# Kernel optimization log

Measured on AMD Instinct MI355X. Metric: run time of the kernel, lower is better.

The kernel has to match this reference:

```python
import jax, jax.numpy as jnp
import numpy as np
from functools import partial

V, BS, L, H, C = 50257, 1024, 6, 12, 768
HD = C // H

def _ln(x, w, b):
    mu = jnp.mean(x, axis=-1, keepdims=True)
    var = jnp.var(x, axis=-1, keepdims=True)
    return (x - mu) * jax.lax.rsqrt(var + 1e-5) * w + b

def setup_inputs() -> dict:
    key = jax.random.key(0)
    ks = jax.random.split(key, 12)
    s = 0.02
    inp = {
        "idx": jax.random.randint(ks[0], (4, 1024), 0, V, dtype=jnp.int32),
        "wte": jax.random.normal(ks[1], (V, C), jnp.float32) * s,
        "wpe": jax.random.normal(ks[2], (BS, C), jnp.float32) * s,
        # per-block stacked params; linear weights stored [in, out]
        "ln1_w": jnp.ones((L, C)), "ln1_b": jnp.zeros((L, C)),
        "attn_w": jax.random.normal(ks[3], (L, C, 3 * C), jnp.float32) * s,
        "attn_b": jnp.zeros((L, 3 * C)),
        "proj_w": jax.random.normal(ks[4], (L, C, C), jnp.float32) * s,
        "proj_b": jnp.zeros((L, C)),
        "ln2_w": jnp.ones((L, C)), "ln2_b": jnp.zeros((L, C)),
        "fc_w": jax.random.normal(ks[5], (L, C, 4 * C), jnp.float32) * s,
        "fc_b": jnp.zeros((L, 4 * C)),
        "fc2_w": jax.random.normal(ks[6], (L, 4 * C, C), jnp.float32) * s,
        "fc2_b": jnp.zeros((L, C)),
        "lnf_w": jnp.ones((C,)), "lnf_b": jnp.zeros((C,)),
    }
    return inp

def _forward(idx, wte, wpe, ln1_w, ln1_b, attn_w, attn_b, proj_w, proj_b,
             ln2_w, ln2_b, fc_w, fc_b, fc2_w, fc2_b, lnf_w, lnf_b):
    B, T = idx.shape
    x = wte[idx] + wpe[:T]  # [B,T,C]
    causal = jnp.tril(jnp.ones((T, T), bool))  # [T,T]
    scale = 1.0 / np.sqrt(HD)
    neg_inf = jnp.finfo(x.dtype).min

    def block(x, p):
        l1w, l1b, aw, ab, pw, pb, l2w, l2b, fw, fb, f2w, f2b = p
        h = _ln(x, l1w, l1b)
        qkv = h @ aw + ab  # [B,T,3C]
        q, k, v = jnp.split(qkv, 3, axis=-1)
        q = q.reshape(B, T, H, HD)
        k = k.reshape(B, T, H, HD)
        v = v.reshape(B, T, H, HD)
        att = jnp.einsum('bqhd,bkhd->bhqk', q, k) * scale
        att = jnp.where(causal, att, neg_inf)
        att = jax.nn.softmax(att, axis=-1)
        y = jnp.einsum('bhqk,bkhd->bqhd', att, v).reshape(B, T, C)
        x = x + y @ pw + pb
        h = _ln(x, l2w, l2b)
        h = jax.nn.gelu(h @ fw + fb, approximate=False)  # torch nn.GELU default = exact
        x = x + h @ f2w + f2b
        return x, None

    params = (ln1_w, ln1_b, attn_w, attn_b, proj_w, proj_b,
              ln2_w, ln2_b, fc_w, fc_b, fc2_w, fc2_b)
    x, _ = jax.lax.scan(block, x, params)
    x = _ln(x, lnf_w, lnf_b)
    logits = x @ wte.T  # tied lm_head, no bias
    return logits

def reference(idx, wte, wpe, ln1_w, ln1_b, attn_w, attn_b, proj_w, proj_b,
              ln2_w, ln2_b, fc_w, fc_b, fc2_w, fc2_b, lnf_w, lnf_b):
    return _forward(idx, wte, wpe, ln1_w, ln1_b, attn_w, attn_b, proj_w, proj_b,
                    ln2_w, ln2_b, fc_w, fc_b, fc2_w, fc2_b, lnf_w, lnf_b)
```

## Files before the change

### kernel.cpp

```cpp
#include <hip/hip_runtime.h>

#define BT     4096
#define CDIM   768
#define NLAYER 6
#define NHEAD  12
#define VREAL  50257
#define VPAD   50432

typedef __bf16 bf16x8 __attribute__((ext_vector_type(8)));
typedef float  f32x4  __attribute__((ext_vector_type(4)));

__device__ __forceinline__ unsigned short f2bf(float f) {
    unsigned int u = __builtin_bit_cast(unsigned int, f);
    u += 0x7fffu + ((u >> 16) & 1u);
    return (unsigned short)(u >> 16);
}

__device__ __forceinline__ void swz_block(int &bx, int &by) {
    int gx = gridDim.x;
    int nwg = gx * gridDim.y;
    if ((nwg & 7) == 0) {
        int lin = by * gx + bx;
        int q = nwg >> 3;
        lin = (lin & 7) * q + (lin >> 3);
        bx = lin % gx;
        by = lin / gx;
    }
}

__global__ __launch_bounds__(256) void transpose_conv(
    const float* __restrict__ in, unsigned short* __restrict__ out, int K, int N)
{
    in  += (size_t)blockIdx.z * K * N;
    out += (size_t)blockIdx.z * K * N;
    __shared__ float t[32][33];
    int j0 = blockIdx.x * 32;
    int i0 = blockIdx.y * 32;
    int c = threadIdx.x;
    int r = threadIdx.y;
    #pragma unroll
    for (int rr = r; rr < 32; rr += 8)
        t[rr][c] = in[(size_t)(i0 + rr) * N + j0 + c];
    __syncthreads();
    #pragma unroll
    for (int rr = r; rr < 32; rr += 8)
        out[(size_t)(j0 + rr) * K + i0 + c] = f2bf(t[c][rr]);
}

__global__ __launch_bounds__(256) void wteconv(
    const float* __restrict__ wte, unsigned short* __restrict__ out)
{
    size_t e = ((size_t)blockIdx.x * 256 + threadIdx.x) * 4;
    int row = (int)(e / CDIM);
    int col = (int)(e % CDIM);
    ushort4 o;
    if (row < VREAL) {
        float4 v = *(const float4*)(wte + (size_t)row * CDIM + col);
        o.x = f2bf(v.x); o.y = f2bf(v.y); o.z = f2bf(v.z); o.w = f2bf(v.w);
    } else {
        o.x = 0; o.y = 0; o.z = 0; o.w = 0;
    }
    *(ushort4*)(out + e) = o;
}

__global__ __launch_bounds__(256) void embed_kernel(
    const int* __restrict__ idx, const float* __restrict__ wte,
    const float* __restrict__ wpe, float* __restrict__ x)
{
    int row = blockIdx.x;
    int t = row & 1023;
    int id = idx[row];
    const float* s = wte + (size_t)id * CDIM;
    const float* p = wpe + (size_t)t * CDIM;
    float* o = x + (size_t)row * CDIM;
    for (int c = threadIdx.x; c < CDIM; c += 256) o[c] = s[c] + p[c];
}

__global__ __launch_bounds__(256) void ln_kernel(
    const float* __restrict__ x, const float* __restrict__ w,
    const float* __restrict__ b, unsigned short* __restrict__ out)
{
    int row = blockIdx.x * 4 + (threadIdx.x >> 6);
    int lane = threadIdx.x & 63;
    const float* xp = x + (size_t)row * CDIM;
    float v[12];
    float s = 0.f, sq = 0.f;
    #pragma unroll
    for (int j = 0; j < 12; ++j) {
        float t = xp[j * 64 + lane];
        v[j] = t; s += t; sq += t * t;
    }
    #pragma unroll
    for (int o = 32; o > 0; o >>= 1) {
        s  += __shfl_xor(s, o, 64);
        sq += __shfl_xor(sq, o, 64);
    }
    float mu  = s * (1.f / CDIM);
    float var = sq * (1.f / CDIM) - mu * mu;
    float rs  = rsqrtf(var + 1e-5f);
    unsigned short* op = out + (size_t)row * CDIM;
    #pragma unroll
    for (int j = 0; j < 12; ++j) {
        int c = j * 64 + lane;
        op[c] = f2bf((v[j] - mu) * rs * w[c] + b[c]);
    }
}

template<int MODE>
__global__ __launch_bounds__(256) void gemm_kernel(
    const unsigned short* __restrict__ A, const unsigned short* __restrict__ Bt,
    const float* __restrict__ bias, const float* __restrict__ resid,
    float* __restrict__ outF, unsigned short* __restrict__ outB,
    unsigned short* __restrict__ qout, unsigned short* __restrict__ kout,
    unsigned short* __restrict__ vtout,
    int K, int Nout)
{
    __shared__ alignas(16) unsigned short As[2][4096];
    __shared__ alignas(16) unsigned short Bs[2][4096];
    const int tid  = threadIdx.x;
    const int wv   = tid >> 6;
    const int lane = tid & 63;
    int bx = blockIdx.x, by = blockIdx.y;
    swz_block(bx, by);
    const int m0 = bx * 128;
    const int n0 = by * 128;
    const int wr = wv >> 1, wc = wv & 1;
    const int srow = lane >> 2;
    const int skk  = (lane & 3) * 8;
    const int fr = lane & 15;
    const int fk = (lane >> 4) * 8;

    auto stage = [&](int k0, int bb) {
        #pragma unroll
        for (int j = 0; j < 2; ++j) {
            int row = j * 64 + wv * 16 + srow;
            const unsigned short* ga = A  + (size_t)(m0 + row) * K + k0 + skk;
            const unsigned short* gb = Bt + (size_t)(n0 + row) * K + k0 + skk;
            __builtin_amdgcn_global_load_lds(
                (const __attribute__((address_space(1))) unsigned int*)ga,
                (__attribute__((address_space(3))) unsigned int*)&As[bb][j * 2048 + wv * 512],
                16, 0, 0);
            __builtin_amdgcn_global_load_lds(
                (const __attribute__((address_space(1))) unsigned int*)gb,
                (__attribute__((address_space(3))) unsigned int*)&Bs[bb][j * 2048 + wv * 512],
                16, 0, 0);
        }
    };

    f32x4 acc[4][4];
    #pragma unroll
    for (int i = 0; i < 4; ++i)
        #pragma unroll
        for (int j = 0; j < 4; ++j) acc[i][j] = f32x4{0.f, 0.f, 0.f, 0.f};

    stage(0, 0);
    __syncthreads();

    const int nt = K >> 5;
    for (int t = 0; t < nt; ++t) {
        const int cb = t & 1;
        if (t + 1 < nt) stage((t + 1) << 5, cb ^ 1);
        bf16x8 a[4], bb[4];
        #pragma unroll
        for (int m = 0; m < 4; ++m)
            a[m] = *(const bf16x8*)&As[cb][(wr * 64 + m * 16 + fr) * 32 + fk];
        #pragma unroll
        for (int n = 0; n < 4; ++n)
            bb[n] = *(const bf16x8*)&Bs[cb][(wc * 64 + n * 16 + fr) * 32 + fk];
        #pragma unroll
        for (int m = 0; m < 4; ++m)
            #pragma unroll
            for (int n = 0; n < 4; ++n)
                acc[m][n] = __builtin_amdgcn_mfma_f32_16x16x32_bf16(
                    a[m], bb[n], acc[m][n], 0, 0, 0);
        __syncthreads();
    }

    const int colb = n0 + wc * 64 + fr;
    const int rowb = m0 + wr * 64 + (lane >> 4) * 4;
    #pragma unroll
    for (int m = 0; m < 4; ++m) {
        #pragma unroll
        for (int n = 0; n < 4; ++n) {
            int col = colb + n * 16;
            int which = col / 768;
            int hh = (col - which * 768) >> 6;
            int dd = col & 63;
            #pragma unroll
            for (int r = 0; r < 4; ++r) {
                int row = rowb + m * 16 + r;
                float v = acc[m][n][r];
                if (MODE == 1) {
                    outF[(size_t)row * Nout + col] =
                        resid[(size_t)row * Nout + col] + v + bias[col];
                } else if (MODE == 2) {
                    float u = v + bias[col];
                    float g = 0.5f * u * (1.f + erff(u * 0.70710678118654752f));
                    outB[(size_t)row * Nout + col] = f2bf(g);
                } else if (MODE == 4) {
                    int bb2 = row >> 10, tt = row & 1023;
                    unsigned short val = f2bf(v + bias[col]);
                    if (which == 0)
                        qout[(((size_t)bb2 * NHEAD + hh) * 1024 + tt) * 64 + dd] = val;
                    else if (which == 1)
                        kout[(((size_t)bb2 * NHEAD + hh) * 1024 + tt) * 64 + dd] = val;
                    else
                        vtout[(((size_t)bb2 * NHEAD + hh) * 64 + dd) * 1024 + tt] = val;
                }
            }
        }
    }
}

__global__ __launch_bounds__(512, 2) void gemm256_kernel(
    const unsigned short* __restrict__ A, const unsigned short* __restrict__ Bt,
    float* __restrict__ outF, int K, int Nout)
{
    __shared__ alignas(16) unsigned short ldsA[2][16384];
    __shared__ alignas(16) unsigned short ldsB[2][16384];
    const int tid  = threadIdx.x;
    const int wid  = tid >> 6;
    const int lane = tid & 63;
    int bx = blockIdx.x, by = blockIdx.y;
    swz_block(bx, by);
    const int m0 = bx * 256;
    const int n0 = by * 256;
    const int wm = wid >> 2;
    const int wn = wid & 3;
    const int srow = wid * 8 + (lane >> 3);
    const int scol = (lane & 7) * 8;
    const int fr = lane & 15;
    const int fg = lane >> 4;

    auto stage = [&](int kt, int bb) {
        const int k0 = kt * 64;
        #pragma unroll
        for (int j = 0; j < 4; ++j) {
            const unsigned short* ga = A  + (size_t)(m0 + j * 64 + srow) * K + k0 + scol;
            const unsigned short* gb = Bt + (size_t)(n0 + j * 64 + srow) * K + k0 + scol;
            __builtin_amdgcn_global_load_lds(
                (const __attribute__((address_space(1))) unsigned int*)ga,
                (__attribute__((address_space(3))) unsigned int*)&ldsA[bb][j * 4096 + wid * 512],
                16, 0, 0);
            __builtin_amdgcn_global_load_lds(
                (const __attribute__((address_space(1))) unsigned int*)gb,
                (__attribute__((address_space(3))) unsigned int*)&ldsB[bb][j * 4096 + wid * 512],
                16, 0, 0);
        }
    };

    f32x4 acc[8][4];
    #pragma unroll
    for (int i = 0; i < 8; ++i)
        #pragma unroll
        for (int j = 0; j < 4; ++j) acc[i][j] = f32x4{0.f, 0.f, 0.f, 0.f};

    stage(0, 0);
    __syncthreads();

    const int nt = K >> 6;
    for (int t = 0; t < nt; ++t) {
        const int cb = t & 1;
        if (t + 1 < nt) stage(t + 1, cb ^ 1);
        #pragma unroll
        for (int ks = 0; ks < 2; ++ks) {
            bf16x8 a[8], b[4];
            #pragma unroll
            for (int m = 0; m < 8; ++m)
                a[m] = *(const bf16x8*)&ldsA[cb][(wm * 128 + m * 16 + fr) * 64 + ks * 32 + fg * 8];
            #pragma unroll
            for (int n = 0; n < 4; ++n)
                b[n] = *(const bf16x8*)&ldsB[cb][(wn * 64 + n * 16 + fr) * 64 + ks * 32 + fg * 8];
            #pragma unroll
            for (int m = 0; m < 8; ++m)
                #pragma unroll
                for (int n = 0; n < 4; ++n)
                    acc[m][n] = __builtin_amdgcn_mfma_f32_16x16x32_bf16(
                        a[m], b[n], acc[m][n], 0, 0, 0);
        }
        __syncthreads();
    }

    const int colb = n0 + wn * 64 + fr;
    const int rowb = m0 + wm * 128 + fg * 4;
    #pragma unroll
    for (int m = 0; m < 8; ++m) {
        #pragma unroll
        for (int n = 0; n < 4; ++n) {
            int col = colb + n * 16;
            if (col < Nout) {
                #pragma unroll
                for (int r = 0; r < 4; ++r) {
                    int row = rowb + m * 16 + r;
                    outF[(size_t)row * Nout + col] = acc[m][n][r];
                }
            }
        }
    }
}

__global__ __launch_bounds__(256) void attn_mfma_kernel(
    const unsigned short* __restrict__ qb, const unsigned short* __restrict__ kb,
    const unsigned short* __restrict__ vtb, unsigned short* __restrict__ y)
{
    __shared__ alignas(16) unsigned short Ps[4][16][72];
    const int qt = 15 - blockIdx.x;
    const int h = blockIdx.y, b = blockIdx.z;
    const int w = threadIdx.x >> 6, lane = threadIdx.x & 63;
    const int fr = lane & 15;
    const int fg = lane >> 4;
    const size_t bh = (size_t)(b * NHEAD + h);
    const unsigned short* Qb = qb  + bh * 1024 * 64;
    const unsigned short* Kb = kb  + bh * 1024 * 64;
    const unsigned short* Vt = vtb + bh * 64 * 1024;
    const int q0 = qt * 64 + w * 16;

    bf16x8 aq[2];
    aq[0] = *(const bf16x8*)(Qb + (size_t)(q0 + fr) * 64 + fg * 8);
    aq[1] = *(const bf16x8*)(Qb + (size_t)(q0 + fr) * 64 + 32 + fg * 8);

    f32x4 o[4];
    #pragma unroll
    for (int c = 0; c < 4; ++c) o[c] = f32x4{0.f, 0.f, 0.f, 0.f};
    float m[4], l[4];
    #pragma unroll
    for (int r = 0; r < 4; ++r) { m[r] = -1e30f; l[r] = 0.f; }

    for (int kt = 0; kt <= qt; ++kt) {
        const unsigned short* Kt = Kb + (size_t)kt * 64 * 64;
        f32x4 s[4];
        #pragma unroll
        for (int c = 0; c < 4; ++c) {
            bf16x8 bk0 = *(const bf16x8*)(Kt + (size_t)(c * 16 + fr) * 64 + fg * 8);
            bf16x8 bk1 = *(const bf16x8*)(Kt + (size_t)(c * 16 + fr) * 64 + 32 + fg * 8);
            s[c] = f32x4{0.f, 0.f, 0.f, 0.f};
            s[c] = __builtin_amdgcn_mfma_f32_16x16x32_bf16(aq[0], bk0, s[c], 0, 0, 0);
            s[c] = __builtin_amdgcn_mfma_f32_16x16x32_bf16(aq[1], bk1, s[c], 0, 0, 0);
        }
        float sc[4][4];
        #pragma unroll
        for (int c = 0; c < 4; ++c)
            #pragma unroll
            for (int r = 0; r < 4; ++r) {
                float v = s[c][r] * 0.125f;
                if (kt == qt && (kt * 64 + c * 16 + fr) > (q0 + fg * 4 + r))
                    v = -1e30f;
                sc[c][r] = v;
            }
        #pragma unroll
        for (int r = 0; r < 4; ++r) {
            float tm = fmaxf(fmaxf(sc[0][r], sc[1][r]), fmaxf(sc[2][r], sc[3][r]));
            tm = fmaxf(tm, __shfl_xor(tm, 1, 64));
            tm = fmaxf(tm, __shfl_xor(tm, 2, 64));
            tm = fmaxf(tm, __shfl_xor(tm, 4, 64));
            tm = fmaxf(tm, __shfl_xor(tm, 8, 64));
            float mn = fmaxf(m[r], tm);
            float corr = __expf(m[r] - mn);
            m[r] = mn;
            float ps = 0.f;
            #pragma unroll
            for (int c = 0; c < 4; ++c) {
                float p = __expf(sc[c][r] - mn);
                sc[c][r] = p;
                ps += p;
            }
            ps += __shfl_xor(ps, 1, 64);
            ps += __shfl_xor(ps, 2, 64);
            ps += __shfl_xor(ps, 4, 64);
            ps += __shfl_xor(ps, 8, 64);
            l[r] = l[r] * corr + ps;
            #pragma unroll
            for (int c = 0; c < 4; ++c) o[c][r] *= corr;
            #pragma unroll
            for (int c = 0; c < 4; ++c)
                Ps[w][fg * 4 + r][c * 16 + fr] = f2bf(sc[c][r]);
        }
        asm volatile("s_waitcnt lgkmcnt(0)" ::: "memory");
        bf16x8 ap0 = *(const bf16x8*)&Ps[w][fr][fg * 8];
        bf16x8 ap1 = *(const bf16x8*)&Ps[w][fr][32 + fg * 8];
        #pragma unroll
        for (int c = 0; c < 4; ++c) {
            const unsigned short* vb = Vt + (size_t)(c * 16 + fr) * 1024 + kt * 64;
            bf16x8 bv0 = *(const bf16x8*)(vb + fg * 8);
            bf16x8 bv1 = *(const bf16x8*)(vb + 32 + fg * 8);
            o[c] = __builtin_amdgcn_mfma_f32_16x16x32_bf16(ap0, bv0, o[c], 0, 0, 0);
            o[c] = __builtin_amdgcn_mfma_f32_16x16x32_bf16(ap1, bv1, o[c], 0, 0, 0);
        }
        asm volatile("s_waitcnt lgkmcnt(0)" ::: "memory");
    }

    float inv[4];
    #pragma unroll
    for (int r = 0; r < 4; ++r) inv[r] = 1.f / l[r];
    #pragma unroll
    for (int c = 0; c < 4; ++c)
        #pragma unroll
        for (int r = 0; r < 4; ++r) {
            int q = q0 + fg * 4 + r;
            y[((size_t)(b * 1024 + q)) * CDIM + h * 64 + c * 16 + fr] =
                f2bf(o[c][r] * inv[r]);
        }
}

extern "C" void kernel_launch(void* const* d_in, const int* in_sizes, int n_in,
                              void* d_out, int out_size, void* d_ws, size_t ws_size,
                              hipStream_t stream) {
    (void)in_sizes; (void)n_in; (void)out_size; (void)ws_size;
    const int*   idx   = (const int*)  d_in[0];
    const float* wte   = (const float*)d_in[1];
    const float* wpe   = (const float*)d_in[2];
    const float* ln1w  = (const float*)d_in[3];
    const float* ln1b  = (const float*)d_in[4];
    const float* attnw = (const float*)d_in[5];
    const float* attnb = (const float*)d_in[6];
    const float* projw = (const float*)d_in[7];
    const float* projb = (const float*)d_in[8];
    const float* ln2w  = (const float*)d_in[9];
    const float* ln2b  = (const float*)d_in[10];
    const float* fcw   = (const float*)d_in[11];
    const float* fcb   = (const float*)d_in[12];
    const float* fc2w  = (const float*)d_in[13];
    const float* fc2b  = (const float*)d_in[14];
    const float* lnfw  = (const float*)d_in[15];
    const float* lnfb  = (const float*)d_in[16];
    float* out = (float*)d_out;

    char* ws = (char*)d_ws;
    size_t off = 0;
    auto alloc = [&](size_t bytes) {
        void* p = ws + off;
        off += (bytes + 255) & ~(size_t)255;
        return p;
    };
    float*          x      = (float*)         alloc((size_t)BT * CDIM * 4);
    unsigned short* hbuf   = (unsigned short*)alloc((size_t)BT * CDIM * 2);
    unsigned short* qbuf   = (unsigned short*)alloc((size_t)BT * CDIM * 2);
    unsigned short* kbuf   = (unsigned short*)alloc((size_t)BT * CDIM * 2);
    unsigned short* vtbuf  = (unsigned short*)alloc((size_t)BT * CDIM * 2);
    unsigned short* ybuf   = (unsigned short*)alloc((size_t)BT * CDIM * 2);
    unsigned short* fcact  = (unsigned short*)alloc((size_t)BT * 4 * CDIM * 2);
    unsigned short* wqkvT  = (unsigned short*)alloc((size_t)NLAYER * 3 * CDIM * CDIM * 2);
    unsigned short* wprojT = (unsigned short*)alloc((size_t)NLAYER * CDIM * CDIM * 2);
    unsigned short* wfcT   = (unsigned short*)alloc((size_t)NLAYER * 4 * CDIM * CDIM * 2);
    unsigned short* wfc2T  = (unsigned short*)alloc((size_t)NLAYER * 4 * CDIM * CDIM * 2);
    unsigned short* wteB   = (unsigned short*)alloc((size_t)VPAD * CDIM * 2);

    transpose_conv<<<dim3(3*CDIM/32,   CDIM/32, NLAYER), dim3(32,8), 0, stream>>>(attnw, wqkvT, CDIM, 3*CDIM);
    transpose_conv<<<dim3(  CDIM/32,   CDIM/32, NLAYER), dim3(32,8), 0, stream>>>(projw, wprojT, CDIM, CDIM);
    transpose_conv<<<dim3(4*CDIM/32,   CDIM/32, NLAYER), dim3(32,8), 0, stream>>>(fcw,  wfcT,  CDIM, 4*CDIM);
    transpose_conv<<<dim3(  CDIM/32, 4*CDIM/32, NLAYER), dim3(32,8), 0, stream>>>(fc2w, wfc2T, 4*CDIM, CDIM);
    wteconv<<<(VPAD * CDIM / 4) / 256, 256, 0, stream>>>(wte, wteB);
    embed_kernel<<<BT, 256, 0, stream>>>(idx, wte, wpe, x);

    for (int l = 0; l < NLAYER; ++l) {
        ln_kernel<<<BT/4, 256, 0, stream>>>(x, ln1w + l*CDIM, ln1b + l*CDIM, hbuf);
        gemm_kernel<4><<<dim3(BT/128, 3*CDIM/128), 256, 0, stream>>>(
            hbuf, wqkvT + (size_t)l*3*CDIM*CDIM, attnb + (size_t)l*3*CDIM,
            nullptr, nullptr, nullptr, qbuf, kbuf, vtbuf, CDIM, 3*CDIM);
        attn_mfma_kernel<<<dim3(16, NHEAD, 4), 256, 0, stream>>>(qbuf, kbuf, vtbuf, ybuf);
        gemm_kernel<1><<<dim3(BT/128, CDIM/128), 256, 0, stream>>>(
            ybuf, wprojT + (size_t)l*CDIM*CDIM, projb + (size_t)l*CDIM,
            x, x, nullptr, nullptr, nullptr, nullptr, CDIM, CDIM);
        ln_kernel<<<BT/4, 256, 0, stream>>>(x, ln2w + l*CDIM, ln2b + l*CDIM, hbuf);
        gemm_kernel<2><<<dim3(BT/128, 4*CDIM/128), 256, 0, stream>>>(
            hbuf, wfcT + (size_t)l*4*CDIM*CDIM, fcb + (size_t)l*4*CDIM,
            nullptr, nullptr, fcact, nullptr, nullptr, nullptr, CDIM, 4*CDIM);
        gemm_kernel<1><<<dim3(BT/128, CDIM/128), 256, 0, stream>>>(
            fcact, wfc2T + (size_t)l*4*CDIM*CDIM, fc2b + (size_t)l*CDIM,
            x, x, nullptr, nullptr, nullptr, nullptr, 4*CDIM, CDIM);
    }
    ln_kernel<<<BT/4, 256, 0, stream>>>(x, lnfw, lnfb, hbuf);
    gemm256_kernel<<<dim3(BT/256, VPAD/256), 512, 0, stream>>>(
        hbuf, wteB, out, CDIM, VREAL);
}
```

Before: 2.451 ms.

## Triple-buffer GEMM LDS staging with explicit vmcnt waits and prefetch distance two

Both GEMM kernels move from double-buffered to triple-buffered LDS staging and issue global-to-LDS loads two K-tiles ahead. The blanket __syncthreads is replaced by explicit s_waitcnt vmcnt counts, raw s_barrier, sched_barrier fences and s_setprio around the MFMA block. The 256 kernel also drops its K-tile from 64 to 32 to fit three buffers in LDS. The goal is to hide global load latency behind MFMA work, at the cost of one barrier per K-step for half as much work in the 256 kernel and hand-counted waits that must match the issued loads.

New measurement: 2.496 ms. No clear change (+1.8%).

```diff
diff --git a/kernel.cpp b/kernel.cpp
--- a/kernel.cpp
+++ b/kernel.cpp
@@ -14,6 +14,12 @@
     unsigned int u = __builtin_bit_cast(unsigned int, f);
     u += 0x7fffu + ((u >> 16) & 1u);
     return (unsigned short)(u >> 16);
+}
+
+__device__ __forceinline__ void gload16(const unsigned short* g, unsigned short* l) {
+    __builtin_amdgcn_global_load_lds(
+        (const __attribute__((address_space(1))) unsigned int*)g,
+        (__attribute__((address_space(3))) unsigned int*)l, 16, 0, 0);
 }
 
 __device__ __forceinline__ void swz_block(int &bx, int &by) {
@@ -115,8 +121,8 @@
     unsigned short* __restrict__ vtout,
     int K, int Nout)
 {
-    __shared__ alignas(16) unsigned short As[2][4096];
-    __shared__ alignas(16) unsigned short Bs[2][4096];
+    __shared__ alignas(16) unsigned short As[3][4096];
+    __shared__ alignas(16) unsigned short Bs[3][4096];
     const int tid  = threadIdx.x;
     const int wv   = tid >> 6;
     const int lane = tid & 63;
@@ -130,20 +136,13 @@
     const int fr = lane & 15;
     const int fk = (lane >> 4) * 8;
 
-    auto stage = [&](int k0, int bb) {
+    auto stage = [&](int t, int bb) {
+        const int k0 = t << 5;
         #pragma unroll
         for (int j = 0; j < 2; ++j) {
             int row = j * 64 + wv * 16 + srow;
-            const unsigned short* ga = A  + (size_t)(m0 + row) * K + k0 + skk;
-            const unsigned short* gb = Bt + (size_t)(n0 + row) * K + k0 + skk;
-            __builtin_amdgcn_global_load_lds(
-                (const __attribute__((address_space(1))) unsigned int*)ga,
-                (__attribute__((address_space(3))) unsigned int*)&As[bb][j * 2048 + wv * 512],
-                16, 0, 0);
-            __builtin_amdgcn_global_load_lds(
-                (const __attribute__((address_space(1))) unsigned int*)gb,
-                (__attribute__((address_space(3))) unsigned int*)&Bs[bb][j * 2048 + wv * 512],
-                16, 0, 0);
+            gload16(A  + (size_t)(m0 + row) * K + k0 + skk, &As[bb][j * 2048 + wv * 512]);
+            gload16(Bt + (size_t)(n0 + row) * K + k0 + skk, &Bs[bb][j * 2048 + wv * 512]);
         }
     };
 
@@ -153,13 +152,18 @@
         #pragma unroll
         for (int j = 0; j < 4; ++j) acc[i][j] = f32x4{0.f, 0.f, 0.f, 0.f};
 
+    const int nt = K >> 5;
     stage(0, 0);
-    __syncthreads();
-
-    const int nt = K >> 5;
+    if (nt > 1) stage(1, 1);
+
     for (int t = 0; t < nt; ++t) {
-        const int cb = t & 1;
-        if (t + 1 < nt) stage((t + 1) << 5, cb ^ 1);
+        const int cb = t % 3;
+        if (t + 2 < nt) stage(t + 2, (t + 2) % 3);
+        if (t + 2 < nt)      asm volatile("s_waitcnt vmcnt(8)" ::: "memory");
+        else if (t + 1 < nt) asm volatile("s_waitcnt vmcnt(4)" ::: "memory");
+        else                 asm volatile("s_waitcnt vmcnt(0)" ::: "memory");
+        __builtin_amdgcn_s_barrier();
+        __builtin_amdgcn_sched_barrier(0);
         bf16x8 a[4], bb[4];
         #pragma unroll
         for (int m = 0; m < 4; ++m)
@@ -167,13 +171,17 @@
         #pragma unroll
         for (int n = 0; n < 4; ++n)
             bb[n] = *(const bf16x8*)&Bs[cb][(wc * 64 + n * 16 + fr) * 32 + fk];
+        __builtin_amdgcn_s_setprio(1);
         #pragma unroll
         for (int m = 0; m < 4; ++m)
             #pragma unroll
             for (int n = 0; n < 4; ++n)
                 acc[m][n] = __builtin_amdgcn_mfma_f32_16x16x32_bf16(
                     a[m], bb[n], acc[m][n], 0, 0, 0);
-        __syncthreads();
+        __builtin_amdgcn_s_setprio(0);
+        asm volatile("s_waitcnt lgkmcnt(0)" ::: "memory");
+        __builtin_amdgcn_sched_barrier(0);
+        __builtin_amdgcn_s_barrier();
     }
 
     const int colb = n0 + wc * 64 + fr;
@@ -216,8 +224,8 @@
     const unsigned short* __restrict__ A, const unsigned short* __restrict__ Bt,
     float* __restrict__ outF, int K, int Nout)
 {
-    __shared__ alignas(16) unsigned short ldsA[2][16384];
-    __shared__ alignas(16) unsigned short ldsB[2][16384];
+    __shared__ alignas(16) unsigned short ldsA[3][8192];
+    __shared__ alignas(16) unsigned short ldsB[3][8192];
     const int tid  = threadIdx.x;
     const int wid  = tid >> 6;
     const int lane = tid & 63;
@@ -227,25 +235,20 @@
     const int n0 = by * 256;
     const int wm = wid >> 2;
     const int wn = wid & 3;
-    const int srow = wid * 8 + (lane >> 3);
-    const int scol = (lane & 7) * 8;
+    const int srow = wid * 16 + (lane >> 2);
+    const int scol = (lane & 3) * 8;
     const int fr = lane & 15;
     const int fg = lane >> 4;
 
-    auto stage = [&](int kt, int bb) {
-        const int k0 = kt * 64;
-        #pragma unroll
-        for (int j = 0; j < 4; ++j) {
-            const unsigned short* ga = A  + (size_t)(m0 + j * 64 + srow) * K + k0 + scol;
-            const unsigned short* gb = Bt + (size_t)(n0 + j * 64 + srow) * K + k0 + scol;
-            __builtin_amdgcn_global_load_lds(
-                (const __attribute__((address_space(1))) unsigned int*)ga,
-                (__attribute__((address_space(3))) unsigned int*)&ldsA[bb][j * 4096 + wid * 512],
-                16, 0, 0);
-            __builtin_amdgcn_global_load_lds(
-                (const __attribute__((address_space(1))) unsigned int*)gb,
-                (__attribute__((address_space(3))) unsigned int*)&ldsB[bb][j * 4096 + wid * 512],
-                16, 0, 0);
+    auto stage = [&](int t, int bb) {
+        const int k0 = t << 5;
+        #pragma unroll
+        for (int j = 0; j < 2; ++j) {
+            int row = j * 128 + srow;
+            gload16(A  + (size_t)(m0 + row) * K + k0 + scol,
+                    &ldsA[bb][(j * 128 + wid * 16) * 32]);
+            gload16(Bt + (size_t)(n0 + row) * K + k0 + scol,
+                    &ldsB[bb][(j * 128 + wid * 16) * 32]);
         }
     };
 
@@ -255,30 +258,36 @@
         #pragma unroll
         for (int j = 0; j < 4; ++j) acc[i][j] = f32x4{0.f, 0.f, 0.f, 0.f};
 
+    const int nt = K >> 5;
     stage(0, 0);
-    __syncthreads();
-
-    const int nt = K >> 6;
+    if (nt > 1) stage(1, 1);
+
     for (int t = 0; t < nt; ++t) {
-        const int cb = t & 1;
-        if (t + 1 < nt) stage(t + 1, cb ^ 1);
-        #pragma unroll
-        for (int ks = 0; ks < 2; ++ks) {
-            bf16x8 a[8], b[4];
-            #pragma unroll
-            for (int m = 0; m < 8; ++m)
-                a[m] = *(const bf16x8*)&ldsA[cb][(wm * 128 + m * 16 + fr) * 64 + ks * 32 + fg * 8];
+        const int cb = t % 3;
+        if (t + 2 < nt) stage(t + 2, (t + 2) % 3);
+        if (t + 2 < nt)      asm volatile("s_waitcnt vmcnt(8)" ::: "memory");
+        else if (t + 1 < nt) asm volatile("s_waitcnt vmcnt(4)" ::: "memory");
+        else                 asm volatile("s_waitcnt vmcnt(0)" ::: "memory");
+        __builtin_amdgcn_s_barrier();
+        __builtin_amdgcn_sched_barrier(0);
+        bf16x8 a[8], b[4];
+        #pragma unroll
+        for (int m = 0; m < 8; ++m)
+            a[m] = *(const bf16x8*)&ldsA[cb][(wm * 128 + m * 16 + fr) * 32 + fg * 8];
+        #pragma unroll
+        for (int n = 0; n < 4; ++n)
+            b[n] = *(const bf16x8*)&ldsB[cb][(wn * 64 + n * 16 + fr) * 32 + fg * 8];
+        __builtin_amdgcn_s_setprio(1);
+        #pragma unroll
+        for (int m = 0; m < 8; ++m)
             #pragma unroll
             for (int n = 0; n < 4; ++n)
-                b[n] = *(const bf16x8*)&ldsB[cb][(wn * 64 + n * 16 + fr) * 64 + ks * 32 + fg * 8];
-            #pragma unroll
-            for (int m = 0; m < 8; ++m)
-                #pragma unroll
-                for (int n = 0; n < 4; ++n)
-                    acc[m][n] = __builtin_amdgcn_mfma_f32_16x16x32_bf16(
-                        a[m], b[n], acc[m][n], 0, 0, 0);
-        }
-        __syncthreads();
+                acc[m][n] = __builtin_amdgcn_mfma_f32_16x16x32_bf16(
+                    a[m], b[n], acc[m][n], 0, 0, 0);
+        __builtin_amdgcn_s_setprio(0);
+        asm volatile("s_waitcnt lgkmcnt(0)" ::: "memory");
+        __builtin_amdgcn_sched_barrier(0);
+        __builtin_amdgcn_s_barrier();
     }
 
     const int colb = n0 + wn * 64 + fr;
```
